# Optimization experiments

Hardware: AMD Instinct MI355X
Metric: run time of the kernel (lower is better)

## Reference

```python
import jax, jax.numpy as jnp
import numpy as np

LEVEL = 3
NUM_BANDS = LEVEL + 1
B, N, D_MODEL, PATCH_NUMS, PRED_LEN = 32, 7, 768, 64, 336

# db4 lowpass decomposition filter (pywt convention)
_DB4_DEC_LO = np.array([
    -0.010597401784997278, 0.032883011666982945, 0.030841381835986965,
    -0.18703481171888114, -0.02798376941698385, 0.6308807679295904,
    0.7148465705525415, 0.23037781330885523], dtype=np.float32)
REC_LO = _DB4_DEC_LO[::-1].copy()                                   # reconstruction lowpass
REC_HI = (_DB4_DEC_LO * ((-1.0) ** (np.arange(8) + 1))).astype(np.float32)  # reconstruction highpass (QMF)


def _upsample2(x):
    # zero-interleave along last axis: (..., L) -> (..., 2L)
    z = jnp.zeros_like(x)
    return jnp.stack([x, z], axis=-1).reshape(*x.shape[:-1], 2 * x.shape[-1])


def _idwt_per(ca, cd, rec_lo, rec_hi):
    # single-level inverse DWT, periodization mode, along last axis: (..., L) -> (..., 2L)
    F = rec_lo.shape[0]
    ua, ud = _upsample2(ca), _upsample2(cd)
    y = jnp.zeros_like(ua)
    for k in range(F):  # small fixed tap loop (F=8)
        y = y + jnp.roll(ua, k, axis=-1) * rec_lo[k] + jnp.roll(ud, k, axis=-1) * rec_hi[k]
    return jnp.roll(y, -(F // 2 - 1), axis=-1)  # compensate filter delay


def _iswt(coeffs, level, rec_lo, rec_hi):
    # coeffs: (..., T, level+1) with bands ordered [cA, cD_level, ..., cD1]
    T = coeffs.shape[-2]
    out = coeffs[..., 0]
    for j in range(level, 0, -1):
        step = 2 ** (j - 1)
        cd = coeffs[..., level - j + 1]
        M = T // step
        # gather the `step` interleaved subsequences as a batch axis: (..., step, M)
        o = jnp.moveaxis(out.reshape(*out.shape[:-1], M, step), -1, -2)
        d = jnp.moveaxis(cd.reshape(*cd.shape[:-1], M, step), -1, -2)
        x1 = _idwt_per(o[..., 0::2], d[..., 0::2], rec_lo, rec_hi)
        x2 = jnp.roll(_idwt_per(o[..., 1::2], d[..., 1::2], rec_lo, rec_hi), 1, axis=-1)
        new = 0.5 * (x1 + x2)  # (..., step, M)
        out = jnp.moveaxis(new, -2, -1).reshape(*out.shape[:-1], T)
    return out


def setup_inputs() -> dict:
    key = jax.random.key(0)
    kx, kw, kb = jax.random.split(key, 3)
    Din = D_MODEL * PATCH_NUMS
    x = jax.random.normal(kx, (B, N, D_MODEL, PATCH_NUMS), dtype=jnp.float32)
    # Linear init ~ U(-1/sqrt(Din), 1/sqrt(Din)); small normal is equivalent for a reference
    W = jax.random.normal(kw, (NUM_BANDS, Din, PRED_LEN), dtype=jnp.float32) * (1.0 / np.sqrt(Din))
    b = jax.random.normal(kb, (NUM_BANDS, PRED_LEN), dtype=jnp.float32) * 0.01
    return {"x": x, "W": W, "b": b}


def reference(x, W, b):
    # x: (B, N, d_model, patch_nums); W: (bands, d_model*patch_nums, pred_len); b: (bands, pred_len)
    Bb, Nn, dm, P = x.shape
    xf = x.reshape(Bb, Nn, dm * P)  # Flatten(start_dim=-2)
    # all band projections as one batched GEMM -> (B, N, pred_len, bands)
    coeffs = jnp.einsum('bnd,kdp->bnpk', xf, W) + b.T
    rec_lo = jnp.asarray(REC_LO)
    rec_hi = jnp.asarray(REC_HI)
    return _iswt(coeffs, LEVEL, rec_lo, rec_hi)  # (B, N, pred_len)
```

## Files before the change

kernel.cpp:

```cpp
#include <hip/hip_runtime.h>
#include <stdint.h>

#define M_ROWS   224
#define K_DIM    49152
#define NCOL     1344
#define PRED     336
#define S_CHUNKS 48
#define STEPS    32

#define XB_OFFSET (32u * 1024u * 1024u)

typedef __attribute__((ext_vector_type(8))) short short8;
typedef __attribute__((ext_vector_type(4))) float floatx4;

__device__ __forceinline__ uint16_t f32_to_bf16(float f) {
    uint32_t u = __builtin_bit_cast(uint32_t, f);
    uint32_t r = (u + 0x7fffu + ((u >> 16) & 1u)) >> 16;
    return (uint16_t)r;
}
__device__ __forceinline__ float bf16_to_f32(uint16_t h) {
    uint32_t u = ((uint32_t)h) << 16;
    return __builtin_bit_cast(float, u);
}
__device__ __forceinline__ uint32_t pack2(float lo, float hi) {
    return (uint32_t)f32_to_bf16(lo) | ((uint32_t)f32_to_bf16(hi) << 16);
}

__global__ __launch_bounds__(256) void cvt_x(
    const float* __restrict__ X, uint16_t* __restrict__ Xb)
{
    const size_t i = ((size_t)blockIdx.x * 256 + threadIdx.x) * 8;
    const float4 a = *(const float4*)(X + i);
    const float4 b = *(const float4*)(X + i + 4);
    uint4 o;
    o.x = pack2(a.x, a.y);
    o.y = pack2(a.z, a.w);
    o.z = pack2(b.x, b.y);
    o.w = pack2(b.z, b.w);
    *(uint4*)(Xb + i) = o;
}

__global__ __launch_bounds__(256, 4) void gemm_partial(
    const uint16_t* __restrict__ Xb,
    const float* __restrict__ W,
    uint16_t* __restrict__ P)
{
    __shared__ uint16_t lA[2][14 * 512];

    const int id = blockIdx.x;
    const int g  = id & 7;
    const int q  = id >> 3;
    const int ct = q % 21;
    const int s  = g + 8 * (q / 21);

    const int tid  = threadIdx.x;
    const int lane = tid & 63;
    const int w    = tid >> 6;
    const int l15  = lane & 15;
    const int kq   = lane >> 4;
    const int c0w  = ct * 64 + w * 16;
    const int band = c0w / PRED;
    const int p0   = c0w - band * PRED;

    const float* wbase = W + (size_t)band * ((size_t)K_DIM * PRED)
                           + (size_t)(kq * 8) * PRED
                           + (size_t)(p0 + l15);
    const size_t grow = (size_t)l15 * K_DIM + (size_t)kq * 8;
    const int kbase = s * (STEPS * 32);

    floatx4 acc[14];
    #pragma unroll
    for (int f = 0; f < 14; ++f) acc[f] = (floatx4){0.f, 0.f, 0.f, 0.f};

    float wcur[8], wnxt[8];

    #pragma unroll
    for (int j = 0; j < 8; ++j) wcur[j] = wbase[(size_t)(kbase + j) * PRED];
    #pragma unroll
    for (int t = 0; t < 4; ++t) {
        const int f = w + 4 * t;
        if (f < 14) {
            const uint16_t* gp = Xb + (size_t)(16 * f) * K_DIM + grow + kbase;
            __builtin_amdgcn_global_load_lds(
                (const __attribute__((address_space(1))) void*)gp,
                (__attribute__((address_space(3))) void*)&lA[0][f * 512],
                16, 0, 0);
        }
    }

    for (int st = 0; st < STEPS; ++st) {
        __syncthreads();
        const int cur = st & 1;

        if (st + 1 < STEPS) {
            const int kn = kbase + (st + 1) * 32;
            #pragma unroll
            for (int t = 0; t < 4; ++t) {
                const int f = w + 4 * t;
                if (f < 14) {
                    const uint16_t* gp = Xb + (size_t)(16 * f) * K_DIM + grow + kn;
                    __builtin_amdgcn_global_load_lds(
                        (const __attribute__((address_space(1))) void*)gp,
                        (__attribute__((address_space(3))) void*)&lA[cur ^ 1][f * 512],
                        16, 0, 0);
                }
            }
            #pragma unroll
            for (int j = 0; j < 8; ++j) wnxt[j] = wbase[(size_t)(kn + j) * PRED];
        }

        short8 bfrag;
        #pragma unroll
        for (int j = 0; j < 4; ++j)
            ((uint32_t*)&bfrag)[j] = pack2(wcur[2 * j], wcur[2 * j + 1]);

        #pragma unroll
        for (int f = 0; f < 14; ++f) {
            short8 afrag = *(const short8*)&lA[cur][f * 512 + lane * 8];
            acc[f] = __builtin_amdgcn_mfma_f32_16x16x32_bf16(afrag, bfrag, acc[f], 0, 0, 0);
        }

        if (st + 1 < STEPS) {
            #pragma unroll
            for (int j = 0; j < 8; ++j) wcur[j] = wnxt[j];
        }
    }

    const int col = c0w + l15;
    #pragma unroll
    for (int f = 0; f < 14; ++f) {
        #pragma unroll
        for (int r = 0; r < 4; ++r) {
            const int m = 16 * f + kq * 4 + r;
            P[((size_t)m * S_CHUNKS + s) * NCOL + col] = f32_to_bf16(acc[f][r]);
        }
    }
}

__device__ const float REC_LO[8] = {
     0.23037781330885523f,  0.7148465705525415f,   0.6308807679295904f,
    -0.02798376941698385f, -0.18703481171888114f,  0.030841381835986965f,
     0.032883011666982945f, -0.010597401784997278f };
__device__ const float REC_HI[8] = {
     0.010597401784997278f, 0.032883011666982945f, -0.030841381835986965f,
    -0.18703481171888114f,  0.02798376941698385f,   0.6308807679295904f,
    -0.7148465705525415f,   0.23037781330885523f };

__global__ __launch_bounds__(1024) void reduce_iswt(
    const uint16_t* __restrict__ P,
    const float* __restrict__ bias,
    float* __restrict__ out)
{
    __shared__ float coeff[NCOL];
    __shared__ float buf[2][PRED];

    const int row = blockIdx.x;
    const int tid = threadIdx.x;
    const uint32_t* pr = (const uint32_t*)(P + (size_t)row * S_CHUNKS * NCOL);

    if (tid < NCOL / 2) {
        float a0 = 0.f, a1 = 0.f;
        #pragma unroll 4
        for (int s = 0; s < S_CHUNKS; ++s) {
            const uint32_t v = pr[s * (NCOL / 2) + tid];
            a0 += bf16_to_f32((uint16_t)(v & 0xffff));
            a1 += bf16_to_f32((uint16_t)(v >> 16));
        }
        coeff[2 * tid]     = a0 + bias[2 * tid];
        coeff[2 * tid + 1] = a1 + bias[2 * tid + 1];
    }
    __syncthreads();

    if (tid < PRED) buf[0][tid] = coeff[tid];
    __syncthreads();

    int curb = 0;
    for (int j = 3; j >= 1; --j) {
        const int step = 1 << (j - 1);
        const int M    = PRED / step;
        const float* cd  = &coeff[(4 - j) * PRED];
        const float* cur = buf[curb];
        float* nxt       = buf[curb ^ 1];
        if (tid < PRED) {
            const int t = tid;
            const int sidx = t & (step - 1);
            const int m = t / step;
            const int mm1 = (m == 0) ? (M - 1) : (m - 1);
            float x1 = 0.f, x2 = 0.f;
            #pragma unroll
            for (int k = 0; k < 8; ++k) {
                int i1 = m + 3 - k;  if (i1 < 0) i1 += M; else if (i1 >= M) i1 -= M;
                if ((i1 & 1) == 0) {
                    const int pos = i1 * step + sidx;
                    x1 += cur[pos] * REC_LO[k] + cd[pos] * REC_HI[k];
                }
                int i2 = mm1 + 3 - k;  if (i2 < 0) i2 += M; else if (i2 >= M) i2 -= M;
                if ((i2 & 1) == 0) {
                    const int pos = (i2 + 1) * step + sidx;
                    x2 += cur[pos] * REC_LO[k] + cd[pos] * REC_HI[k];
                }
            }
            nxt[t] = 0.5f * (x1 + x2);
        }
        __syncthreads();
        curb ^= 1;
    }

    if (tid < PRED) out[(size_t)row * PRED + tid] = buf[curb][tid];
}

extern "C" void kernel_launch(void* const* d_in, const int* in_sizes, int n_in,
                              void* d_out, int out_size, void* d_ws, size_t ws_size,
                              hipStream_t stream) {
    const float* X    = (const float*)d_in[0];
    const float* W    = (const float*)d_in[1];
    const float* bias = (const float*)d_in[2];
    float* out        = (float*)d_out;
    uint16_t* P       = (uint16_t*)d_ws;
    uint16_t* Xb      = (uint16_t*)((char*)d_ws + XB_OFFSET);

    cvt_x       <<<5376, 256, 0, stream>>>(X, Xb);
    gemm_partial<<<21 * S_CHUNKS, 256, 0, stream>>>(Xb, W, P);
    reduce_iswt <<<M_ROWS, 1024, 0, stream>>>(P, bias, out);
}
```

Before: 428.3 us.

## Split GEMM rows across waves with register-direct A loads and separate reduction

The GEMM block grows to 8 waves arranged as 2 row-halves by 4 column groups. Each wave loads its A fragments straight from global memory into registers, dropping the LDS staging and per-step barriers. The K split is halved to 24 chunks of 64 steps, which shrinks the partial-sum buffer. The cross-chunk reduction moves into its own wide kernel that writes fp32 coefficients, and a lighter per-row ISWT kernel follows. The trade-offs are fewer blocks in the GEMM, W fragments now loaded twice per block (once per row-half), and one extra kernel launch plus an fp32 intermediate buffer.

```diff
diff --git a/kernel.cpp b/kernel.cpp
--- a/kernel.cpp
+++ b/kernel.cpp
@@ -5,9 +5,10 @@
 #define K_DIM    49152
 #define NCOL     1344
 #define PRED     336
-#define S_CHUNKS 48
-#define STEPS    32
-
+#define S_CHUNKS 24
+#define STEPS    64
+
+#define C_OFFSET  (16u * 1024u * 1024u)
 #define XB_OFFSET (32u * 1024u * 1024u)
 
 typedef __attribute__((ext_vector_type(8))) short short8;
@@ -40,13 +41,11 @@
     *(uint4*)(Xb + i) = o;
 }
 
-__global__ __launch_bounds__(256, 4) void gemm_partial(
+__global__ __launch_bounds__(512, 4) void gemm_partial(
     const uint16_t* __restrict__ Xb,
     const float* __restrict__ W,
     uint16_t* __restrict__ P)
 {
-    __shared__ uint16_t lA[2][14 * 512];
-
     const int id = blockIdx.x;
     const int g  = id & 7;
     const int q  = id >> 3;
@@ -55,58 +54,46 @@
 
     const int tid  = threadIdx.x;
     const int lane = tid & 63;
-    const int w    = tid >> 6;
+    const int wv   = tid >> 6;
+    const int wm   = wv >> 2;
+    const int wn   = wv & 3;
     const int l15  = lane & 15;
     const int kq   = lane >> 4;
-    const int c0w  = ct * 64 + w * 16;
+
+    const int c0w  = ct * 64 + wn * 16;
     const int band = c0w / PRED;
     const int p0   = c0w - band * PRED;
-
-    const float* wbase = W + (size_t)band * ((size_t)K_DIM * PRED)
-                           + (size_t)(kq * 8) * PRED
-                           + (size_t)(p0 + l15);
-    const size_t grow = (size_t)l15 * K_DIM + (size_t)kq * 8;
     const int kbase = s * (STEPS * 32);
 
-    floatx4 acc[14];
-    #pragma unroll
-    for (int f = 0; f < 14; ++f) acc[f] = (floatx4){0.f, 0.f, 0.f, 0.f};
-
-    float wcur[8], wnxt[8];
-
-    #pragma unroll
-    for (int j = 0; j < 8; ++j) wcur[j] = wbase[(size_t)(kbase + j) * PRED];
-    #pragma unroll
-    for (int t = 0; t < 4; ++t) {
-        const int f = w + 4 * t;
-        if (f < 14) {
-            const uint16_t* gp = Xb + (size_t)(16 * f) * K_DIM + grow + kbase;
-            __builtin_amdgcn_global_load_lds(
-                (const __attribute__((address_space(1))) void*)gp,
-                (__attribute__((address_space(3))) void*)&lA[0][f * 512],
-                16, 0, 0);
-        }
-    }
-
+    const float* wp = W + (size_t)band * ((size_t)K_DIM * PRED)
+                        + (size_t)(kbase + kq * 8) * PRED
+                        + (size_t)(p0 + l15);
+    const uint16_t* ap = Xb + (size_t)(wm * 112 + l15) * K_DIM + kbase + kq * 8;
+
+    floatx4 acc[7];
+    #pragma unroll
+    for (int f = 0; f < 7; ++f) acc[f] = (floatx4){0.f, 0.f, 0.f, 0.f};
+
+    short8 acur[7], anxt[7];
+    float  wcur[8], wnxt[8];
+
+    #pragma unroll
+    for (int f = 0; f < 7; ++f)
+        acur[f] = *(const short8*)(ap + (size_t)(16 * f) * K_DIM);
+    #pragma unroll
+    for (int j = 0; j < 8; ++j)
+        wcur[j] = wp[(size_t)j * PRED];
+
+    #pragma unroll 2
     for (int st = 0; st < STEPS; ++st) {
-        __syncthreads();
-        const int cur = st & 1;
-
         if (st + 1 < STEPS) {
-            const int kn = kbase + (st + 1) * 32;
-            #pragma unroll
-            for (int t = 0; t < 4; ++t) {
-                const int f = w + 4 * t;
-                if (f < 14) {
-                    const uint16_t* gp = Xb + (size_t)(16 * f) * K_DIM + grow + kn;
-                    __builtin_amdgcn_global_load_lds(
-                        (const __attribute__((address_space(1))) void*)gp,
-                        (__attribute__((address_space(3))) void*)&lA[cur ^ 1][f * 512],
-                        16, 0, 0);
-                }
-            }
-            #pragma unroll
-            for (int j = 0; j < 8; ++j) wnxt[j] = wbase[(size_t)(kn + j) * PRED];
+            const int ko = (st + 1) * 32;
+            #pragma unroll
+            for (int f = 0; f < 7; ++f)
+                anxt[f] = *(const short8*)(ap + (size_t)(16 * f) * K_DIM + ko);
+            #pragma unroll
+            for (int j = 0; j < 8; ++j)
+                wnxt[j] = wp[(size_t)(ko + j) * PRED];
         }
 
         short8 bfrag;
@@ -115,26 +102,41 @@
             ((uint32_t*)&bfrag)[j] = pack2(wcur[2 * j], wcur[2 * j + 1]);
 
         #pragma unroll
-        for (int f = 0; f < 14; ++f) {
-            short8 afrag = *(const short8*)&lA[cur][f * 512 + lane * 8];
-            acc[f] = __builtin_amdgcn_mfma_f32_16x16x32_bf16(afrag, bfrag, acc[f], 0, 0, 0);
-        }
+        for (int f = 0; f < 7; ++f)
+            acc[f] = __builtin_amdgcn_mfma_f32_16x16x32_bf16(acur[f], bfrag, acc[f], 0, 0, 0);
 
         if (st + 1 < STEPS) {
             #pragma unroll
+            for (int f = 0; f < 7; ++f) acur[f] = anxt[f];
+            #pragma unroll
             for (int j = 0; j < 8; ++j) wcur[j] = wnxt[j];
         }
     }
 
     const int col = c0w + l15;
     #pragma unroll
-    for (int f = 0; f < 14; ++f) {
+    for (int f = 0; f < 7; ++f) {
         #pragma unroll
         for (int r = 0; r < 4; ++r) {
-            const int m = 16 * f + kq * 4 + r;
+            const int m = wm * 112 + 16 * f + kq * 4 + r;
             P[((size_t)m * S_CHUNKS + s) * NCOL + col] = f32_to_bf16(acc[f][r]);
         }
     }
+}
+
+__global__ __launch_bounds__(256) void reduce_partials(
+    const uint16_t* __restrict__ P,
+    const float* __restrict__ bias,
+    float* __restrict__ C)
+{
+    const int t   = blockIdx.x * 256 + threadIdx.x;
+    const int row = t / NCOL;
+    const int col = t - row * NCOL;
+    const uint16_t* p = P + (size_t)row * S_CHUNKS * NCOL + col;
+    float a = bias[col];
+    #pragma unroll
+    for (int s = 0; s < S_CHUNKS; ++s) a += bf16_to_f32(p[s * NCOL]);
+    C[t] = a;
 }
 
 __device__ const float REC_LO[8] = {
@@ -146,9 +148,8 @@
     -0.18703481171888114f,  0.02798376941698385f,   0.6308807679295904f,
     -0.7148465705525415f,   0.23037781330885523f };
 
-__global__ __launch_bounds__(1024) void reduce_iswt(
-    const uint16_t* __restrict__ P,
-    const float* __restrict__ bias,
+__global__ __launch_bounds__(512) void iswt_rows(
+    const float* __restrict__ C,
     float* __restrict__ out)
 {
     __shared__ float coeff[NCOL];
@@ -156,19 +157,8 @@
 
     const int row = blockIdx.x;
     const int tid = threadIdx.x;
-    const uint32_t* pr = (const uint32_t*)(P + (size_t)row * S_CHUNKS * NCOL);
-
-    if (tid < NCOL / 2) {
-        float a0 = 0.f, a1 = 0.f;
-        #pragma unroll 4
-        for (int s = 0; s < S_CHUNKS; ++s) {
-            const uint32_t v = pr[s * (NCOL / 2) + tid];
-            a0 += bf16_to_f32((uint16_t)(v & 0xffff));
-            a1 += bf16_to_f32((uint16_t)(v >> 16));
-        }
-        coeff[2 * tid]     = a0 + bias[2 * tid];
-        coeff[2 * tid + 1] = a1 + bias[2 * tid + 1];
-    }
+
+    for (int c = tid; c < NCOL; c += 512) coeff[c] = C[(size_t)row * NCOL + c];
     __syncthreads();
 
     if (tid < PRED) buf[0][tid] = coeff[tid];
@@ -217,9 +207,11 @@
     const float* bias = (const float*)d_in[2];
     float* out        = (float*)d_out;
     uint16_t* P       = (uint16_t*)d_ws;
+    float*    C       = (float*)((char*)d_ws + C_OFFSET);
     uint16_t* Xb      = (uint16_t*)((char*)d_ws + XB_OFFSET);
 
-    cvt_x       <<<5376, 256, 0, stream>>>(X, Xb);
-    gemm_partial<<<21 * S_CHUNKS, 256, 0, stream>>>(Xb, W, P);
-    reduce_iswt <<<M_ROWS, 1024, 0, stream>>>(P, bias, out);
-}
+    cvt_x          <<<5376, 256, 0, stream>>>(X, Xb);
+    gemm_partial   <<<21 * S_CHUNKS, 512, 0, stream>>>(Xb, W, P);
+    reduce_partials<<<1176, 256, 0, stream>>>(P, bias, C);
+    iswt_rows      <<<M_ROWS, 512, 0, stream>>>(C, out);
+}
```

Result: slower. 586.0 us (+36.8%).
